# Kernel tuning notes

Hardware: AMD Instinct MI355X
Metric: run time of the kernel (lower is better)

## Reference

```python
import jax, jax.numpy as jnp
import numpy as np

# Involution2D config (matches init_kwargs)
F = 256          # filters
K = 3            # kernel_size
G = 16           # groups
RR = 4           # reduce_ratio
BN_EPS = 1e-3    # keras BatchNormalization default epsilon


def setup_inputs() -> dict:
    key = jax.random.key(0)
    ks = jax.random.split(key, 8)
    C = 256
    Cr = F // RR                    # reduce_mapping channels = 64
    KKG = K * K * G                 # span_mapping channels = 144
    s = lambda k, sh, fan: jax.random.normal(k, sh, jnp.float32) * (1.0 / np.sqrt(fan))
    return {
        "x": jax.random.normal(ks[0], (4, 128, 128, C), jnp.float32),
        # reduce_mapping: 1x1 conv + BN(inference) + relu
        "Wr": s(ks[1], (C, Cr), C),
        "br": jnp.zeros((Cr,), jnp.float32),
        "gamma": jnp.ones((Cr,), jnp.float32),
        "beta": jnp.zeros((Cr,), jnp.float32),
        "mean": jax.random.normal(ks[2], (Cr,), jnp.float32) * 0.1,
        "var": jax.random.uniform(ks[3], (Cr,), jnp.float32, 0.5, 1.5),
        # span_mapping: 1x1 conv -> K*K*G dynamic weights
        "Ws": s(ks[4], (Cr, KKG), Cr),
        "bs": jnp.zeros((KKG,), jnp.float32),
        # initial_mapping: 1x1 conv -> F (applied since F != K*K*G)
        "Wi": s(ks[5], (C, F), C),
        "bi": jnp.zeros((F,), jnp.float32),
    }


def reference(x, Wr, br, gamma, beta, mean, var, Ws, bs, Wi, bi):
    B, H, W, _ = x.shape
    KK = K * K
    # reduce_mapping: 1x1 conv + BN(inference) + relu
    r = jnp.einsum('bhwc,cd->bhwd', x, Wr) + br
    r = jax.nn.relu((r - mean) * jax.lax.rsqrt(var + BN_EPS) * gamma + beta)
    # span_mapping: per-pixel dynamic kernel weights [B,H,W,KK*G] -> [B,H,W,G,1,KK]
    w = jnp.einsum('bhwd,dk->bhwk', r, Ws) + bs
    w = w.reshape(B, H, W, G, KK)[:, :, :, :, None, :]
    # initial_mapping: 1x1 conv -> F channels
    xi = jnp.einsum('bhwc,cf->bhwf', x, Wi) + bi
    # tf.image.extract_patches (SAME, stride=1, rate=1): layout is
    # (kernel_pos major, channel minor), i.e. flat index = kpos*F + c
    pad = (K - 1) // 2
    xp = jnp.pad(xi, ((0, 0), (pad, pad), (pad, pad), (0, 0)))
    patches = jnp.stack(
        [xp[:, i:i + H, j:j + W, :] for i in range(K) for j in range(K)],
        axis=3)                                   # [B,H,W,KK,F]
    # faithful to the original K.reshape of the flat [KK*F] axis
    patches = patches.reshape(B, H, W, G, F // G, KK)
    out = jnp.sum(w * patches, axis=-1)           # [B,H,W,G,F//G]
    return out.reshape(B, H, W, F)
```

## Files before the change

kernel.cpp:

```cpp
#include <hip/hip_runtime.h>

#define BN_EPS 1e-3f

typedef __attribute__((ext_vector_type(8))) short bf16x8;
typedef __attribute__((ext_vector_type(4))) float f32x4;

__device__ inline unsigned short f2b(float f) {
    unsigned int u = __float_as_uint(f);
    unsigned int r = (u + 0x7fffu + ((u >> 16) & 1u)) >> 16;
    return (unsigned short)r;
}
__device__ inline float b2f(unsigned short h) {
    return __uint_as_float(((unsigned int)h) << 16);
}

__global__ void k_prep(const float* __restrict__ Wi, const float* __restrict__ Wr,
                       const float* __restrict__ Ws,
                       unsigned short* __restrict__ Bt, unsigned short* __restrict__ Wst) {
    int t = blockIdx.x * 256 + threadIdx.x;
    if (t < 320 * 256) {
        int n = t >> 8, k = t & 255;
        float v = (n < 256) ? Wi[k * 256 + n] : Wr[k * 64 + (n - 256)];
        Bt[t] = f2b(v);
    } else {
        int t2 = t - 320 * 256;
        if (t2 < 144 * 64) {
            int n = t2 >> 6, k = t2 & 63;
            Wst[t2] = f2b(Ws[k * 144 + n]);
        }
    }
}

#define AXIP 264
#define ARS_OFF (64 * AXIP)
#define ASMN (ARS_OFF + 64 * 72)

__global__ __launch_bounds__(256, 3) void k_xiw(
    const float* __restrict__ x, const unsigned short* __restrict__ Bt,
    const unsigned short* __restrict__ Wst,
    const float* __restrict__ bi, const float* __restrict__ br,
    const float* __restrict__ gamma, const float* __restrict__ beta,
    const float* __restrict__ mean, const float* __restrict__ var,
    const float* __restrict__ bs,
    unsigned short* __restrict__ xi_g, unsigned short* __restrict__ w_g)
{
    __shared__ __attribute__((aligned(16))) unsigned short sm[ASMN];
    const int tid = threadIdx.x;
    const long long px0 = (long long)blockIdx.x * 64;

    const int wv = tid >> 6;
    const int lane = tid & 63;
    const int col = lane & 15;
    const int quad = lane >> 4;

#pragma unroll
    for (int it = 0; it < 8; ++it) {
        const int flat = it * 256 + tid;
        const int px = flat >> 5;
        const int cho = (flat & 31) * 8;
        const float* src = x + (px0 + px) * 256 + cho;
        float4 v0 = *(const float4*)&src[0];
        float4 v1 = *(const float4*)&src[4];
        int4 pk;
        pk.x = (int)((unsigned)f2b(v0.x) | ((unsigned)f2b(v0.y) << 16));
        pk.y = (int)((unsigned)f2b(v0.z) | ((unsigned)f2b(v0.w) << 16));
        pk.z = (int)((unsigned)f2b(v1.x) | ((unsigned)f2b(v1.y) << 16));
        pk.w = (int)((unsigned)f2b(v1.z) | ((unsigned)f2b(v1.w) << 16));
        *(int4*)&sm[px * AXIP + cho] = pk;
    }
    __syncthreads();

    f32x4 acc[5][4];
#pragma unroll
    for (int jj = 0; jj < 5; ++jj)
#pragma unroll
        for (int m = 0; m < 4; ++m) acc[jj][m] = (f32x4){0.f, 0.f, 0.f, 0.f};

#pragma unroll
    for (int kc = 0; kc < 8; ++kc) {
        const int kb = kc * 32 + quad * 8;
        bf16x8 a[4];
#pragma unroll
        for (int m = 0; m < 4; ++m)
            a[m] = *(const bf16x8*)&sm[(m * 16 + col) * AXIP + kb];
#pragma unroll
        for (int jj = 0; jj < 5; ++jj) {
            const int j = wv * 5 + jj;
            bf16x8 b = *(const bf16x8*)&Bt[(j * 16 + col) * 256 + kb];
#pragma unroll
            for (int m = 0; m < 4; ++m)
                acc[jj][m] = __builtin_amdgcn_mfma_f32_16x16x32_bf16(a[m], b, acc[jj][m], 0, 0, 0);
        }
    }
    __syncthreads();

#pragma unroll
    for (int jj = 0; jj < 5; ++jj) {
        const int j = wv * 5 + jj;
        if (j < 16) {
            const int n = j * 16 + col;
            const float bv = bi[n];
#pragma unroll
            for (int m = 0; m < 4; ++m)
#pragma unroll
                for (int rg = 0; rg < 4; ++rg) {
                    const int row = m * 16 + quad * 4 + rg;
                    sm[row * AXIP + n] = f2b(acc[jj][m][rg] + bv);
                }
        } else {
            const int d = (j - 16) * 16 + col;
            const float sc = gamma[d] * rsqrtf(var[d] + BN_EPS);
            const float bb2 = (br[d] - mean[d]) * sc + beta[d];
#pragma unroll
            for (int m = 0; m < 4; ++m)
#pragma unroll
                for (int rg = 0; rg < 4; ++rg) {
                    const int row = m * 16 + quad * 4 + rg;
                    const float v = acc[jj][m][rg] * sc + bb2;
                    sm[ARS_OFF + row * 72 + d] = f2b(fmaxf(v, 0.f));
                }
        }
    }
    __syncthreads();

    f32x4 wa[9];
#pragma unroll
    for (int j = 0; j < 9; ++j) wa[j] = (f32x4){0.f, 0.f, 0.f, 0.f};
#pragma unroll
    for (int kc = 0; kc < 2; ++kc) {
        const int kb = kc * 32 + quad * 8;
        bf16x8 ra = *(const bf16x8*)&sm[ARS_OFF + (wv * 16 + col) * 72 + kb];
#pragma unroll
        for (int j = 0; j < 9; ++j) {
            bf16x8 wb = *(const bf16x8*)&Wst[(j * 16 + col) * 64 + kb];
            wa[j] = __builtin_amdgcn_mfma_f32_16x16x32_bf16(ra, wb, wa[j], 0, 0, 0);
        }
    }

#pragma unroll
    for (int it = 0; it < 8; ++it) {
        const int flat = it * 256 + tid;
        const int px = flat >> 5;
        const int cho = (flat & 31) * 8;
        int4 v = *(const int4*)&sm[px * AXIP + cho];
        *(int4*)&xi_g[(px0 + px) * 256 + cho] = v;
    }

#pragma unroll
    for (int j = 0; j < 9; ++j) {
        const int n = j * 16 + col;
        const float bv = bs[n];
#pragma unroll
        for (int rg = 0; rg < 4; ++rg) {
            const int row = wv * 16 + quad * 4 + rg;
            w_g[(px0 + row) * 144 + n] = f2b(wa[j][rg] + bv);
        }
    }
}

#define GXIP 264
#define GWL_OFF (100 * GXIP)
#define GSMN (GWL_OFF + 64 * 144)

__global__ __launch_bounds__(512, 4) void k_gather(
    const unsigned short* __restrict__ xi_g, const unsigned short* __restrict__ w_g,
    float* __restrict__ out)
{
    __shared__ __attribute__((aligned(16))) unsigned short sm[GSMN];
    const int tid = threadIdx.x;
    const int b = blockIdx.x;
    const int bx = (b & 7) * 128 + (b >> 3);
    const int w0 = (bx & 15) * 8;
    const int h0 = ((bx >> 4) & 15) * 8;
    const int bb = bx >> 8;

#pragma unroll
    for (int it = 0; it < 7; ++it) {
        const int flat = it * 512 + tid;
        if (flat < 3200) {
            const int px = flat >> 5;
            const int cho = (flat & 31) * 8;
            const int hr = px / 10, hc = px - hr * 10;
            const int gh = h0 - 1 + hr, gw = w0 - 1 + hc;
            int4 v;
            if (((unsigned)gh < 128u) && ((unsigned)gw < 128u)) {
                const long long pxg = ((long long)(bb * 128 + gh)) * 128 + gw;
                v = *(const int4*)&xi_g[pxg * 256 + cho];
            } else {
                v = (int4){0, 0, 0, 0};
            }
            *(int4*)&sm[px * GXIP + cho] = v;
        }
    }
#pragma unroll
    for (int it = 0; it < 3; ++it) {
        const int flat = it * 512 + tid;
        if (flat < 1152) {
            const int px = flat / 18;
            const int cho = (flat - px * 18) * 8;
            const long long pxg =
                ((long long)(bb * 128 + h0 + (px >> 3))) * 128 + (w0 + (px & 7));
            int4 v = *(const int4*)&w_g[pxg * 144 + cho];
            *(int4*)&sm[GWL_OFF + px * 144 + cho] = v;
        }
    }
    __syncthreads();

    {
        const int g = tid & 15;
        const int pb = tid >> 4;

        const int idx0 = g * 144;
        const int kp0  = idx0 >> 8;
        const int c0   = idx0 & 255;
        int len1 = 256 - c0; if (len1 > 144) len1 = 144;
        const int kp1  = kp0 + 1;
        const int koff0 = (kp0 / 3) * 10 + (kp0 % 3);
        const int koff1 = (kp1 <= 8) ? ((kp1 / 3) * 10 + (kp1 % 3)) : 0;

#pragma unroll
        for (int jj = 0; jj < 2; ++jj) {
            const int p = pb + 32 * jj;
            const int phb = (p >> 3) * 10 + (p & 7);
            const int base0 = (phb + koff0) * GXIP + c0;
            const int base1 = (phb + koff1) * GXIP;

            float wf[9];
#pragma unroll
            for (int kk = 0; kk < 9; ++kk)
                wf[kk] = b2f(sm[GWL_OFF + p * 144 + g * 9 + kk]);

            float res[16];
            {
                int4 xv[9];
#pragma unroll
                for (int i = 0; i < 9; ++i) {
                    const int e = i * 8;
                    const int addr = (e < len1) ? (base0 + e) : (base1 + (e - len1));
                    xv[i] = *(const int4*)&sm[addr];
                }
#pragma unroll
                for (int f2 = 0; f2 < 8; ++f2) {
                    float a = 0.f;
#pragma unroll
                    for (int kk = 0; kk < 9; ++kk) {
                        const int e = f2 * 9 + kk;
                        const int word = ((const int*)&xv[e >> 3])[(e >> 1) & 3];
                        const unsigned short u = (e & 1) ? (unsigned short)(((unsigned)word) >> 16)
                                                         : (unsigned short)(word & 0xffff);
                        a += wf[kk] * b2f(u);
                    }
                    res[f2] = a;
                }
            }
            {
                int4 xv[9];
#pragma unroll
                for (int i = 9; i < 18; ++i) {
                    const int e = i * 8;
                    const int addr = (e < len1) ? (base0 + e) : (base1 + (e - len1));
                    xv[i - 9] = *(const int4*)&sm[addr];
                }
#pragma unroll
                for (int f2 = 8; f2 < 16; ++f2) {
                    float a = 0.f;
#pragma unroll
                    for (int kk = 0; kk < 9; ++kk) {
                        const int e = f2 * 9 + kk;
                        const int i = (e >> 3) - 9;
                        const int word = ((const int*)&xv[i])[(e >> 1) & 3];
                        const unsigned short u = (e & 1) ? (unsigned short)(((unsigned)word) >> 16)
                                                         : (unsigned short)(word & 0xffff);
                        a += wf[kk] * b2f(u);
                    }
                    res[f2] = a;
                }
            }

            const long long orow =
                (((long long)(bb * 128 + h0 + (p >> 3))) * 128 + (w0 + (p & 7))) * 256 + g * 16;
#pragma unroll
            for (int q = 0; q < 4; ++q) {
                float4 o = {res[q * 4 + 0], res[q * 4 + 1], res[q * 4 + 2], res[q * 4 + 3]};
                *(float4*)&out[orow + q * 4] = o;
            }
        }
    }
}

extern "C" void kernel_launch(void* const* d_in, const int* in_sizes, int n_in,
                              void* d_out, int out_size, void* d_ws, size_t ws_size,
                              hipStream_t stream) {
    const float* x     = (const float*)d_in[0];
    const float* Wr    = (const float*)d_in[1];
    const float* br    = (const float*)d_in[2];
    const float* gamma = (const float*)d_in[3];
    const float* beta  = (const float*)d_in[4];
    const float* mean  = (const float*)d_in[5];
    const float* var   = (const float*)d_in[6];
    const float* Ws    = (const float*)d_in[7];
    const float* bs    = (const float*)d_in[8];
    const float* Wi    = (const float*)d_in[9];
    const float* bi    = (const float*)d_in[10];
    float* out = (float*)d_out;

    unsigned char* ws = (unsigned char*)d_ws;
    unsigned short* Bt   = (unsigned short*)(ws + 0);
    unsigned short* Wst  = (unsigned short*)(ws + 163840);
    unsigned short* xi_g = (unsigned short*)(ws + 182272);
    unsigned short* w_g  = (unsigned short*)(ws + 33736704);

    k_prep<<<dim3(356), dim3(256), 0, stream>>>(Wi, Wr, Ws, Bt, Wst);
    k_xiw<<<dim3(1024), dim3(256), 0, stream>>>(
        x, Bt, Wst, bi, br, gamma, beta, mean, var, bs, xi_g, w_g);
    k_gather<<<dim3(1024), dim3(512), 0, stream>>>(xi_g, w_g, out);
}
```

Baseline: 196.3 us.

## Double k_xiw tile to 128 pixels with 8 waves and write xi directly from registers

Result: no change. 198.1 us (+0.9%).

```diff
diff --git a/kernel.cpp b/kernel.cpp
--- a/kernel.cpp
+++ b/kernel.cpp
@@ -32,10 +32,10 @@
 }
 
 #define AXIP 264
-#define ARS_OFF (64 * AXIP)
-#define ASMN (ARS_OFF + 64 * 72)
-
-__global__ __launch_bounds__(256, 3) void k_xiw(
+#define ASMN (128 * AXIP)
+#define ARSP 72
+
+__global__ __launch_bounds__(512, 4) void k_xiw(
     const float* __restrict__ x, const unsigned short* __restrict__ Bt,
     const unsigned short* __restrict__ Wst,
     const float* __restrict__ bi, const float* __restrict__ br,
@@ -46,16 +46,18 @@
 {
     __shared__ __attribute__((aligned(16))) unsigned short sm[ASMN];
     const int tid = threadIdx.x;
-    const long long px0 = (long long)blockIdx.x * 64;
+    const long long px0 = (long long)blockIdx.x * 128;
 
     const int wv = tid >> 6;
     const int lane = tid & 63;
     const int col = lane & 15;
     const int quad = lane >> 4;
+    const int mh = wv >> 2;
+    const int nq = wv & 3;
 
 #pragma unroll
     for (int it = 0; it < 8; ++it) {
-        const int flat = it * 256 + tid;
+        const int flat = it * 512 + tid;
         const int px = flat >> 5;
         const int cho = (flat & 31) * 8;
         const float* src = x + (px0 + px) * 256 + cho;
@@ -82,10 +84,10 @@
         bf16x8 a[4];
 #pragma unroll
         for (int m = 0; m < 4; ++m)
-            a[m] = *(const bf16x8*)&sm[(m * 16 + col) * AXIP + kb];
+            a[m] = *(const bf16x8*)&sm[(mh * 64 + m * 16 + col) * AXIP + kb];
 #pragma unroll
         for (int jj = 0; jj < 5; ++jj) {
-            const int j = wv * 5 + jj;
+            const int j = nq * 5 + jj;
             bf16x8 b = *(const bf16x8*)&Bt[(j * 16 + col) * 256 + kb];
 #pragma unroll
             for (int m = 0; m < 4; ++m)
@@ -96,29 +98,30 @@
 
 #pragma unroll
     for (int jj = 0; jj < 5; ++jj) {
-        const int j = wv * 5 + jj;
+        const int j = nq * 5 + jj;
         if (j < 16) {
             const int n = j * 16 + col;
             const float bv = bi[n];
 #pragma unroll
-            for (int m = 0; m < 4; ++m)
-#pragma unroll
-                for (int rg = 0; rg < 4; ++rg) {
-                    const int row = m * 16 + quad * 4 + rg;
-                    sm[row * AXIP + n] = f2b(acc[jj][m][rg] + bv);
-                }
+            for (int m = 0; m < 4; ++m) {
+                const long long pxb = px0 + mh * 64 + m * 16 + quad * 4;
+#pragma unroll
+                for (int rg = 0; rg < 4; ++rg)
+                    xi_g[(pxb + rg) * 256 + n] = f2b(acc[jj][m][rg] + bv);
+            }
         } else {
             const int d = (j - 16) * 16 + col;
             const float sc = gamma[d] * rsqrtf(var[d] + BN_EPS);
             const float bb2 = (br[d] - mean[d]) * sc + beta[d];
 #pragma unroll
-            for (int m = 0; m < 4; ++m)
+            for (int m = 0; m < 4; ++m) {
+                const int rowb = mh * 64 + m * 16 + quad * 4;
 #pragma unroll
                 for (int rg = 0; rg < 4; ++rg) {
-                    const int row = m * 16 + quad * 4 + rg;
                     const float v = acc[jj][m][rg] * sc + bb2;
-                    sm[ARS_OFF + row * 72 + d] = f2b(fmaxf(v, 0.f));
-                }
+                    sm[(rowb + rg) * ARSP + d] = f2b(fmaxf(v, 0.f));
+                }
+            }
         }
     }
     __syncthreads();
@@ -129,32 +132,21 @@
 #pragma unroll
     for (int kc = 0; kc < 2; ++kc) {
         const int kb = kc * 32 + quad * 8;
-        bf16x8 ra = *(const bf16x8*)&sm[ARS_OFF + (wv * 16 + col) * 72 + kb];
+        bf16x8 ra = *(const bf16x8*)&sm[(wv * 16 + col) * ARSP + kb];
 #pragma unroll
         for (int j = 0; j < 9; ++j) {
             bf16x8 wb = *(const bf16x8*)&Wst[(j * 16 + col) * 64 + kb];
             wa[j] = __builtin_amdgcn_mfma_f32_16x16x32_bf16(ra, wb, wa[j], 0, 0, 0);
         }
     }
-
-#pragma unroll
-    for (int it = 0; it < 8; ++it) {
-        const int flat = it * 256 + tid;
-        const int px = flat >> 5;
-        const int cho = (flat & 31) * 8;
-        int4 v = *(const int4*)&sm[px * AXIP + cho];
-        *(int4*)&xi_g[(px0 + px) * 256 + cho] = v;
-    }
-
 #pragma unroll
     for (int j = 0; j < 9; ++j) {
         const int n = j * 16 + col;
         const float bv = bs[n];
-#pragma unroll
-        for (int rg = 0; rg < 4; ++rg) {
-            const int row = wv * 16 + quad * 4 + rg;
-            w_g[(px0 + row) * 144 + n] = f2b(wa[j][rg] + bv);
-        }
+        const long long pxb = px0 + wv * 16 + quad * 4;
+#pragma unroll
+        for (int rg = 0; rg < 4; ++rg)
+            w_g[(pxb + rg) * 144 + n] = f2b(wa[j][rg] + bv);
     }
 }
 
@@ -311,7 +303,7 @@
     unsigned short* w_g  = (unsigned short*)(ws + 33736704);
 
     k_prep<<<dim3(356), dim3(256), 0, stream>>>(Wi, Wr, Ws, Bt, Wst);
-    k_xiw<<<dim3(1024), dim3(256), 0, stream>>>(
+    k_xiw<<<dim3(512), dim3(512), 0, stream>>>(
         x, Bt, Wst, bi, br, gamma, beta, mean, var, bs, xi_g, w_g);
     k_gather<<<dim3(1024), dim3(512), 0, stream>>>(xi_g, w_g, out);
 }
```
